# Optimization experiments

Hardware: AMD Instinct MI355X
Metric: run time of the kernel (lower is better)

Reference implementation:

```python
import jax, jax.numpy as jnp
import numpy as np

NEG_SLOPE = 0.2  # PyG GATConv default negative_slope


def setup_inputs() -> dict:
    key = jax.random.key(0)
    k1, k2, k3, k4, k5 = jax.random.split(key, 5)
    N, E, IN, H, C = 50000, 800000, 128, 4, 64
    x = jax.random.normal(k1, (N, IN), dtype=jnp.float32)
    edge_index = jax.random.randint(k2, (2, E), 0, N, dtype=jnp.int32)
    W = jax.random.normal(k3, (IN, H * C), dtype=jnp.float32) * (1.0 / np.sqrt(IN))
    att_src = jax.random.normal(k4, (H, C), dtype=jnp.float32) * 0.1
    att_dst = jax.random.normal(k5, (H, C), dtype=jnp.float32) * 0.1
    bias = jnp.zeros((C,), dtype=jnp.float32)
    return {"x": x, "edge_index": edge_index, "W": W,
            "att_src": att_src, "att_dst": att_dst, "bias": bias}


def reference(x, edge_index, W, att_src, att_dst, bias):
    N = x.shape[0]
    H, C = att_src.shape
    # add self loops (PyG GATConv default add_self_loops=True)
    loop = jnp.arange(N, dtype=edge_index.dtype)
    src = jnp.concatenate([edge_index[0], loop])  # message source j
    dst = jnp.concatenate([edge_index[1], loop])  # message target i
    # linear projection, per-head view [N, H, C]
    h = (x @ W).reshape(N, H, C)
    # per-node attention terms [N, H]
    a_src = jnp.einsum('nhc,hc->nh', h, att_src)
    a_dst = jnp.einsum('nhc,hc->nh', h, att_dst)
    # per-edge logits with leaky relu [Etot, H]
    e = jax.nn.leaky_relu(a_src[src] + a_dst[dst], NEG_SLOPE)
    # segment softmax over incoming edges of each destination node
    emax = jax.ops.segment_max(e, dst, num_segments=N)       # [N, H]
    ex = jnp.exp(e - emax[dst])                              # [Etot, H]
    denom = jax.ops.segment_sum(ex, dst, num_segments=N)     # [N, H]
    alpha = ex / denom[dst]                                  # [Etot, H]
    # weighted scatter-aggregate of source features
    msg = h[src] * alpha[:, :, None]                         # [Etot, H, C]
    out = jax.ops.segment_sum(msg, dst, num_segments=N)      # [N, H, C]
    # concat=False -> mean over heads, then bias, then module-level ELU
    out = out.mean(axis=1) + bias
    return jax.nn.elu(out)
```

## Files before the change

### kernel.cpp

```cpp
#include <hip/hip_runtime.h>

#define NEG_SLOPE 0.2f
static constexpr int IN_F = 128;
static constexpr int NHEAD = 4;
static constexpr int CH = 64;
static constexpr int HC = 256;
static constexpr int SC_EPB = 2000;
static constexpr int CB_CAP = 6144;

static __host__ size_t align256(size_t v) { return (v + 255) & ~((size_t)255); }

__device__ inline ushort f2bf(float f) {
    unsigned u = __float_as_uint(f);
    unsigned r = u + 0x7FFFu + ((u >> 16) & 1u);
    return (ushort)(r >> 16);
}
__device__ inline float bf2f(ushort s) { return __uint_as_float(((unsigned)s) << 16); }

typedef short s16x8 __attribute__((ext_vector_type(8)));
typedef float f32x16 __attribute__((ext_vector_type(16)));

__global__ __launch_bounds__(256) void prep_kernel(
    const float* __restrict__ W, ushort* __restrict__ Wt,
    int* __restrict__ coarse_cnt)
{
    int f = blockIdx.x * 256 + threadIdx.x;
    int k = f >> 8;
    int n = f & 255;
    Wt[n * IN_F + k] = f2bf(W[(size_t)k * HC + n]);
    if (blockIdx.x == 0) coarse_cnt[threadIdx.x] = 0;
}

__global__ __launch_bounds__(256) void gemm_mfma_kernel(
    const float* __restrict__ x, const ushort* __restrict__ Wt,
    const float* __restrict__ att_src, const float* __restrict__ att_dst,
    ushort* __restrict__ hb, float* __restrict__ a_src, float* __restrict__ a_dst,
    const int* __restrict__ dst, int* __restrict__ coarse_cnt,
    int E, int epb, int NTB, int NB, int N)
{
    constexpr int LDK = 136;
    __shared__ ushort As[64 * LDK];
    __shared__ ushort Bs[128 * LDK];
    ushort* Hs = As;

    const int t = threadIdx.x;

    if (blockIdx.x >= NTB) {
        int* hist = (int*)As;
        hist[t] = 0;
        __syncthreads();
        int slice = (blockIdx.x - NTB) * 2 + blockIdx.y;
        int lo = slice * epb;
        int hi = min(E, lo + epb);
        for (int i = lo + t; i < hi; i += 256)
            atomicAdd(&hist[((unsigned)dst[i]) >> 8], 1);
        __syncthreads();
        if (t < NB && hist[t]) atomicAdd(&coarse_cnt[t], hist[t]);
        return;
    }

    const int m0 = blockIdx.x * 64;
    const int n0 = blockIdx.y * 128;

    #pragma unroll
    for (int u = 0; u < 8; ++u) {
        int f = t + 256 * u;
        int r = f >> 5;
        int k4 = (f & 31) * 4;
        int row = m0 + r;
        float4 v = make_float4(0.f, 0.f, 0.f, 0.f);
        if (row < N) v = *(const float4*)(x + (size_t)row * IN_F + k4);
        ushort4 o;
        o.x = f2bf(v.x); o.y = f2bf(v.y); o.z = f2bf(v.z); o.w = f2bf(v.w);
        *(ushort4*)&As[r * LDK + k4] = o;
    }
    #pragma unroll
    for (int u = 0; u < 8; ++u) {
        int f = t + 256 * u;
        int n = f >> 4;
        int k8 = (f & 15) * 8;
        uint4 v = *(const uint4*)(Wt + (size_t)(n0 + n) * IN_F + k8);
        *(uint4*)&Bs[n * LDK + k8] = v;
    }
    __syncthreads();

    const int w = t >> 6;
    const int lane = t & 63;
    const int mrow = 32 * (w >> 1) + (lane & 31);
    const int nbase = 64 * (w & 1) + (lane & 31);
    const int kq = (lane >> 5) * 8;

    f32x16 acc0 = {}, acc1 = {};
    #pragma unroll
    for (int s = 0; s < 8; ++s) {
        s16x8 af = *(const s16x8*)&As[mrow * LDK + 16 * s + kq];
        s16x8 b0 = *(const s16x8*)&Bs[nbase * LDK + 16 * s + kq];
        s16x8 b1 = *(const s16x8*)&Bs[(nbase + 32) * LDK + 16 * s + kq];
        acc0 = __builtin_amdgcn_mfma_f32_32x32x16_bf16(af, b0, acc0, 0, 0, 0);
        acc1 = __builtin_amdgcn_mfma_f32_32x32x16_bf16(af, b1, acc1, 0, 0, 0);
    }
    __syncthreads();

    {
        int rbase = 4 * (lane >> 5) + 32 * (w >> 1);
        int c0 = 64 * (w & 1) + (lane & 31);
        #pragma unroll
        for (int r = 0; r < 16; ++r) {
            int rowL = rbase + (r & 3) + 8 * (r >> 2);
            Hs[rowL * LDK + c0]      = f2bf(acc0[r]);
            Hs[rowL * LDK + c0 + 32] = f2bf(acc1[r]);
        }
    }
    __syncthreads();

    {
        int r2 = t >> 2;
        int q = t & 3;
        int row = m0 + r2;
        uint4 p0 = *(const uint4*)&Hs[r2 * LDK + 32 * q];
        uint4 p1 = *(const uint4*)&Hs[r2 * LDK + 32 * q + 8];
        uint4 p2 = *(const uint4*)&Hs[r2 * LDK + 32 * q + 16];
        uint4 p3 = *(const uint4*)&Hs[r2 * LDK + 32 * q + 24];
        if (row < N) {
            ushort* dsth = hb + (size_t)row * HC + n0 + 32 * q;
            *(uint4*)(dsth)      = p0;
            *(uint4*)(dsth + 8)  = p1;
            *(uint4*)(dsth + 16) = p2;
            *(uint4*)(dsth + 24) = p3;
        }
        int hq = 2 * blockIdx.y + (q >> 1);
        int cb = (q & 1) * 32;
        const float* asp = att_src + hq * CH + cb;
        const float* adp = att_dst + hq * CH + cb;
        unsigned uu[16] = { p0.x, p0.y, p0.z, p0.w, p1.x, p1.y, p1.z, p1.w,
                            p2.x, p2.y, p2.z, p2.w, p3.x, p3.y, p3.z, p3.w };
        float ps = 0.f, pd = 0.f;
        #pragma unroll
        for (int i = 0; i < 16; ++i) {
            float lo = bf2f((ushort)(uu[i] & 0xFFFFu));
            float hi = bf2f((ushort)(uu[i] >> 16));
            ps += lo * asp[2 * i] + hi * asp[2 * i + 1];
            pd += lo * adp[2 * i] + hi * adp[2 * i + 1];
        }
        ps += __shfl_xor(ps, 1, 64);
        pd += __shfl_xor(pd, 1, 64);
        if ((q & 1) == 0 && row < N) {
            a_src[(size_t)row * NHEAD + hq] = ps;
            a_dst[(size_t)row * NHEAD + hq] = pd;
        }
    }
}

__global__ __launch_bounds__(256) void scan_coarse(
    const int* __restrict__ coarse_cnt, int* __restrict__ ebase,
    int* __restrict__ bucket_cur, int* __restrict__ rowptr,
    int NB, int N, int E)
{
    __shared__ int sm[256];
    int t = threadIdx.x;
    int v = (t < NB) ? coarse_cnt[t] : 0;
    sm[t] = v;
    __syncthreads();
    #pragma unroll
    for (int off = 1; off < 256; off <<= 1) {
        int a = sm[t];
        int b = (t >= off) ? sm[t - off] : 0;
        __syncthreads();
        sm[t] = a + b;
        __syncthreads();
    }
    int incl = sm[t];
    int excl = incl - v;
    if (t < NB) { ebase[t] = excl; bucket_cur[t] = excl; }
    if (t == NB - 1) ebase[NB] = incl;
    if (t == 0) rowptr[N] = E + N;
}

__global__ __launch_bounds__(256) void bucket_scatter(
    const int* __restrict__ src, const int* __restrict__ dst,
    int* __restrict__ bucket_cur, unsigned* __restrict__ ebuf,
    int E, int NB)
{
    __shared__ int hist[256];
    __shared__ int lbase[256];
    __shared__ int gbase[256];
    __shared__ int cur[256];
    __shared__ unsigned sbuf[SC_EPB + 48];
    __shared__ unsigned char tb[SC_EPB + 48];
    int t = threadIdx.x;
    int lo = blockIdx.x * SC_EPB;
    int hi = min(E, lo + SC_EPB);
    int cnt = hi - lo;
    hist[t] = 0;
    __syncthreads();
    unsigned pk[8]; int bk[8];
    #pragma unroll
    for (int u = 0; u < 8; ++u) {
        int i = lo + t + 256 * u;
        bk[u] = -1;
        if (i < hi) {
            unsigned d = (unsigned)dst[i];
            bk[u] = (int)(d >> 8);
            pk[u] = (((unsigned)src[i]) << 8) | (d & 255u);
            atomicAdd(&hist[bk[u]], 1);
        }
    }
    __syncthreads();
    int v = hist[t];
    lbase[t] = v;
    __syncthreads();
    #pragma unroll
    for (int off = 1; off < 256; off <<= 1) {
        int a = lbase[t];
        int b = (t >= off) ? lbase[t - off] : 0;
        __syncthreads();
        lbase[t] = a + b;
        __syncthreads();
    }
    int excl = lbase[t] - v;
    if (v) gbase[t] = atomicAdd(&bucket_cur[t], v);
    __syncthreads();
    lbase[t] = excl;
    cur[t] = excl;
    __syncthreads();
    #pragma unroll
    for (int u = 0; u < 8; ++u) {
        if (bk[u] >= 0) {
            int p = atomicAdd(&cur[bk[u]], 1);
            sbuf[p] = pk[u];
            tb[p] = (unsigned char)bk[u];
        }
    }
    __syncthreads();
    for (int j = t; j < cnt; j += 256) {
        int b = tb[j];
        ebuf[gbase[b] + j - lbase[b]] = sbuf[j];
    }
}

__global__ __launch_bounds__(256) void csr_build(
    const unsigned* __restrict__ ebuf, const int* __restrict__ ebase,
    int* __restrict__ rowptr, int* __restrict__ csr_src, int N)
{
    __shared__ int hist[256];
    __shared__ int scn[256];
    __shared__ int cur[256];
    __shared__ unsigned srt[CB_CAP];
    int b = blockIdx.x;
    int t = threadIdx.x;
    int n0 = b << 8;
    int ncnt = min(256, N - n0);
    int lo = ebase[b], hi = ebase[b + 1];
    int cnt = hi - lo;
    int cb = lo + n0;
    hist[t] = 0;
    __syncthreads();
    for (int i = lo + t; i < hi; i += 256)
        atomicAdd(&hist[ebuf[i] & 255u], 1);
    __syncthreads();
    int v = hist[t];
    scn[t] = v;
    __syncthreads();
    #pragma unroll
    for (int off = 1; off < 256; off <<= 1) {
        int a = scn[t];
        int bb = (t >= off) ? scn[t - off] : 0;
        __syncthreads();
        scn[t] = a + bb;
        __syncthreads();
    }
    int excl = scn[t] - v;
    if (t < ncnt) {
        int segstart = cb + excl + t;
        rowptr[n0 + t] = segstart;
        csr_src[segstart] = n0 + t;
    }
    cur[t] = excl;
    __syncthreads();
    if (cnt <= CB_CAP) {
        for (int i = lo + t; i < hi; i += 256) {
            unsigned e = ebuf[i];
            int p = atomicAdd(&cur[e & 255u], 1);
            srt[p] = e;
        }
        __syncthreads();
        for (int j = t; j < cnt; j += 256) {
            unsigned e = srt[j];
            csr_src[cb + j + (int)(e & 255u) + 1] = (int)(e >> 8);
        }
    } else {
        for (int i = lo + t; i < hi; i += 256) {
            unsigned e = ebuf[i];
            int ln = (int)(e & 255u);
            int p = atomicAdd(&cur[ln], 1);
            csr_src[cb + p + ln + 1] = (int)(e >> 8);
        }
    }
}

__global__ __launch_bounds__(256) void aggregate_kernel(
    const ushort* __restrict__ hb, const float* __restrict__ a_src,
    const float* __restrict__ a_dst, const int* __restrict__ rowptr,
    const int* __restrict__ csr_src, const float* __restrict__ bias,
    float* __restrict__ out, int N)
{
    int node = (int)((blockIdx.x * (size_t)blockDim.x + threadIdx.x) >> 6);
    int l = threadIdx.x & 63;
    if (node >= N) return;
    int start = rowptr[node];
    int end = rowptr[node + 1];
    int hd = l >> 4;
    float adh = a_dst[(size_t)node * NHEAD + hd];

    float4 acc0 = make_float4(0.f, 0.f, 0.f, 0.f);
    float4 acc1 = make_float4(0.f, 0.f, 0.f, 0.f);
    float4 acc2 = make_float4(0.f, 0.f, 0.f, 0.f);
    float4 acc3 = make_float4(0.f, 0.f, 0.f, 0.f);
    float s0 = 0.f, s1 = 0.f, s2 = 0.f, s3 = 0.f;

    int k = start;
    for (; k + 4 <= end; k += 4) {
        int sj0 = csr_src[k];
        int sj1 = csr_src[k + 1];
        int sj2 = csr_src[k + 2];
        int sj3 = csr_src[k + 3];
        float a0 = a_src[(size_t)sj0 * NHEAD + hd];
        float a1 = a_src[(size_t)sj1 * NHEAD + hd];
        float a2 = a_src[(size_t)sj2 * NHEAD + hd];
        float a3 = a_src[(size_t)sj3 * NHEAD + hd];
        ushort4 h0 = *(const ushort4*)(hb + ((size_t)sj0 << 8) + 4 * l);
        ushort4 h1 = *(const ushort4*)(hb + ((size_t)sj1 << 8) + 4 * l);
        ushort4 h2 = *(const ushort4*)(hb + ((size_t)sj2 << 8) + 4 * l);
        ushort4 h3 = *(const ushort4*)(hb + ((size_t)sj3 << 8) + 4 * l);
        float e0 = a0 + adh; e0 = fmaxf(e0, NEG_SLOPE * e0); float w0 = __expf(e0);
        float e1 = a1 + adh; e1 = fmaxf(e1, NEG_SLOPE * e1); float w1 = __expf(e1);
        float e2 = a2 + adh; e2 = fmaxf(e2, NEG_SLOPE * e2); float w2 = __expf(e2);
        float e3 = a3 + adh; e3 = fmaxf(e3, NEG_SLOPE * e3); float w3 = __expf(e3);
        s0 += w0; s1 += w1; s2 += w2; s3 += w3;
        acc0.x += w0 * bf2f(h0.x); acc0.y += w0 * bf2f(h0.y);
        acc0.z += w0 * bf2f(h0.z); acc0.w += w0 * bf2f(h0.w);
        acc1.x += w1 * bf2f(h1.x); acc1.y += w1 * bf2f(h1.y);
        acc1.z += w1 * bf2f(h1.z); acc1.w += w1 * bf2f(h1.w);
        acc2.x += w2 * bf2f(h2.x); acc2.y += w2 * bf2f(h2.y);
        acc2.z += w2 * bf2f(h2.z); acc2.w += w2 * bf2f(h2.w);
        acc3.x += w3 * bf2f(h3.x); acc3.y += w3 * bf2f(h3.y);
        acc3.z += w3 * bf2f(h3.z); acc3.w += w3 * bf2f(h3.w);
    }
    for (; k < end; ++k) {
        int sj0 = csr_src[k];
        float a0 = a_src[(size_t)sj0 * NHEAD + hd];
        ushort4 h0 = *(const ushort4*)(hb + ((size_t)sj0 << 8) + 4 * l);
        float e0 = a0 + adh; e0 = fmaxf(e0, NEG_SLOPE * e0);
        float w0 = __expf(e0);
        s0 += w0;
        acc0.x += w0 * bf2f(h0.x); acc0.y += w0 * bf2f(h0.y);
        acc0.z += w0 * bf2f(h0.z); acc0.w += w0 * bf2f(h0.w);
    }

    float inv = 1.0f / (s0 + s1 + s2 + s3);
    float4 acc;
    acc.x = (acc0.x + acc1.x + acc2.x + acc3.x) * inv;
    acc.y = (acc0.y + acc1.y + acc2.y + acc3.y) * inv;
    acc.z = (acc0.z + acc1.z + acc2.z + acc3.z) * inv;
    acc.w = (acc0.w + acc1.w + acc2.w + acc3.w) * inv;

    #pragma unroll
    for (int off = 16; off < 64; off <<= 1) {
        acc.x += __shfl_xor(acc.x, off, 64);
        acc.y += __shfl_xor(acc.y, off, 64);
        acc.z += __shfl_xor(acc.z, off, 64);
        acc.w += __shfl_xor(acc.w, off, 64);
    }
    if (l < 16) {
        float4 b4 = *(const float4*)(bias + 4 * l);
        float4 o;
        o.x = acc.x * 0.25f + b4.x;
        o.y = acc.y * 0.25f + b4.y;
        o.z = acc.z * 0.25f + b4.z;
        o.w = acc.w * 0.25f + b4.w;
        o.x = (o.x > 0.f) ? o.x : (__expf(o.x) - 1.f);
        o.y = (o.y > 0.f) ? o.y : (__expf(o.y) - 1.f);
        o.z = (o.z > 0.f) ? o.z : (__expf(o.z) - 1.f);
        o.w = (o.w > 0.f) ? o.w : (__expf(o.w) - 1.f);
        *(float4*)(out + (size_t)node * CH + 4 * l) = o;
    }
}

extern "C" void kernel_launch(void* const* d_in, const int* in_sizes, int n_in,
                              void* d_out, int out_size, void* d_ws, size_t ws_size,
                              hipStream_t stream)
{
    const float* x         = (const float*)d_in[0];
    const int*   edge_idx  = (const int*)d_in[1];
    const float* W         = (const float*)d_in[2];
    const float* att_src   = (const float*)d_in[3];
    const float* att_dst   = (const float*)d_in[4];
    const float* bias      = (const float*)d_in[5];
    float* out = (float*)d_out;

    const int N = in_sizes[0] / IN_F;
    const int E = in_sizes[1] / 2;
    const int Etot = E + N;
    const int NB = (N + 255) >> 8;
    const int* srcp = edge_idx;
    const int* dstp = edge_idx + E;

    char* ws = (char*)d_ws;
    size_t off = 0;
    ushort*  hb     = (ushort*)(ws + off);   off += align256((size_t)N * HC * sizeof(ushort));
    ushort*  Wt     = (ushort*)(ws + off);   off += align256((size_t)HC * IN_F * sizeof(ushort));
    float*   a_src  = (float*)(ws + off);    off += align256((size_t)N * NHEAD * sizeof(float));
    float*   a_dst  = (float*)(ws + off);    off += align256((size_t)N * NHEAD * sizeof(float));
    int*     ccnt   = (int*)(ws + off);      off += align256(256 * sizeof(int));
    int*     ebase  = (int*)(ws + off);      off += align256(257 * sizeof(int));
    int*     bcur   = (int*)(ws + off);      off += align256(256 * sizeof(int));
    unsigned* ebuf  = (unsigned*)(ws + off); off += align256((size_t)E * sizeof(unsigned));
    int*     rowptr = (int*)(ws + off);      off += align256(((size_t)N + 1) * sizeof(int));
    int*     csrs   = (int*)(ws + off);      off += align256((size_t)Etot * sizeof(int));
    (void)ws_size; (void)n_in; (void)out_size;

    const int NTB = (N + 63) / 64;
    const int PBC = 208;
    const int epbc = (E + 2 * PBC - 1) / (2 * PBC);
    const int PBS = (E + SC_EPB - 1) / SC_EPB;

    prep_kernel<<<IN_F * HC / 256, 256, 0, stream>>>(W, Wt, ccnt);
    dim3 gg(NTB + PBC, 2);
    gemm_mfma_kernel<<<gg, 256, 0, stream>>>(x, Wt, att_src, att_dst, hb,
                                             a_src, a_dst, dstp, ccnt,
                                             E, epbc, NTB, NB, N);
    scan_coarse<<<1, 256, 0, stream>>>(ccnt, ebase, bcur, rowptr, NB, N, E);
    bucket_scatter<<<PBS, 256, 0, stream>>>(srcp, dstp, bcur, ebuf, E, NB);
    csr_build<<<NB, 256, 0, stream>>>(ebuf, ebase, rowptr, csrs, N);
    aggregate_kernel<<<((size_t)N * 64 + 255) / 256, 256, 0, stream>>>(
        hb, a_src, a_dst, rowptr, csrs, bias, out, N);
}
```

Before: 203.8 us.

## Precompute fp16 edge attention weights in CSR build and drop scan kernel

Removes the single-block scan_coarse launch by having bucket_scatter and csr_build each redo the 256-entry scan of the coarse counts. csr_build now also computes each edge's exponentiated leaky-relu logits for all four heads, stores them as fp16 alongside csr_src, and accumulates per-node softmax denominators with shared atomics, writing their reciprocals. The aggregate kernel then reads precomputed weights and the inverse denominator instead of gathering a_src and computing exp per edge per lane. This trades a launch and redundant exp work for an extra 8-byte-per-edge weight array and shared float atomics. It also adds fp16 precision risk, since there is no max subtraction and exp values could overflow fp16.

```diff
diff --git a/kernel.cpp b/kernel.cpp
--- a/kernel.cpp
+++ b/kernel.cpp
@@ -16,19 +16,32 @@
     return (ushort)(r >> 16);
 }
 __device__ inline float bf2f(ushort s) { return __uint_as_float(((unsigned)s) << 16); }
+__device__ inline ushort f2h(float f) {
+    _Float16 h = (_Float16)f;
+    return *(ushort*)&h;
+}
+__device__ inline float h2f(ushort u) {
+    _Float16 h = *(_Float16*)&u;
+    return (float)h;
+}
 
 typedef short s16x8 __attribute__((ext_vector_type(8)));
 typedef float f32x16 __attribute__((ext_vector_type(16)));
 
 __global__ __launch_bounds__(256) void prep_kernel(
     const float* __restrict__ W, ushort* __restrict__ Wt,
-    int* __restrict__ coarse_cnt)
+    int* __restrict__ ccnt, int* __restrict__ cur0,
+    int* __restrict__ rowptr, int N, int Etot)
 {
     int f = blockIdx.x * 256 + threadIdx.x;
     int k = f >> 8;
     int n = f & 255;
     Wt[n * IN_F + k] = f2bf(W[(size_t)k * HC + n]);
-    if (blockIdx.x == 0) coarse_cnt[threadIdx.x] = 0;
+    if (blockIdx.x == 0) {
+        ccnt[threadIdx.x] = 0;
+        cur0[threadIdx.x] = 0;
+        if (threadIdx.x == 0) rowptr[N] = Etot;
+    }
 }
 
 __global__ __launch_bounds__(256) void gemm_mfma_kernel(
@@ -151,36 +164,12 @@
     }
 }
 
-__global__ __launch_bounds__(256) void scan_coarse(
-    const int* __restrict__ coarse_cnt, int* __restrict__ ebase,
-    int* __restrict__ bucket_cur, int* __restrict__ rowptr,
-    int NB, int N, int E)
-{
-    __shared__ int sm[256];
-    int t = threadIdx.x;
-    int v = (t < NB) ? coarse_cnt[t] : 0;
-    sm[t] = v;
-    __syncthreads();
-    #pragma unroll
-    for (int off = 1; off < 256; off <<= 1) {
-        int a = sm[t];
-        int b = (t >= off) ? sm[t - off] : 0;
-        __syncthreads();
-        sm[t] = a + b;
-        __syncthreads();
-    }
-    int incl = sm[t];
-    int excl = incl - v;
-    if (t < NB) { ebase[t] = excl; bucket_cur[t] = excl; }
-    if (t == NB - 1) ebase[NB] = incl;
-    if (t == 0) rowptr[N] = E + N;
-}
-
 __global__ __launch_bounds__(256) void bucket_scatter(
     const int* __restrict__ src, const int* __restrict__ dst,
-    int* __restrict__ bucket_cur, unsigned* __restrict__ ebuf,
-    int E, int NB)
+    const int* __restrict__ ccnt, int* __restrict__ cur0,
+    unsigned* __restrict__ ebuf, int E)
 {
+    __shared__ int eb[256];
     __shared__ int hist[256];
     __shared__ int lbase[256];
     __shared__ int gbase[256];
@@ -188,6 +177,21 @@
     __shared__ unsigned sbuf[SC_EPB + 48];
     __shared__ unsigned char tb[SC_EPB + 48];
     int t = threadIdx.x;
+    int cv = ccnt[t];
+    eb[t] = cv;
+    __syncthreads();
+    #pragma unroll
+    for (int off = 1; off < 256; off <<= 1) {
+        int a = eb[t];
+        int b = (t >= off) ? eb[t - off] : 0;
+        __syncthreads();
+        eb[t] = a + b;
+        __syncthreads();
+    }
+    int myebase = eb[t] - cv;
+    __syncthreads();
+    eb[t] = myebase;
+
     int lo = blockIdx.x * SC_EPB;
     int hi = min(E, lo + SC_EPB);
     int cnt = hi - lo;
@@ -218,7 +222,7 @@
         __syncthreads();
     }
     int excl = lbase[t] - v;
-    if (v) gbase[t] = atomicAdd(&bucket_cur[t], v);
+    if (v) gbase[t] = eb[t] + atomicAdd(&cur0[t], v);
     __syncthreads();
     lbase[t] = excl;
     cur[t] = excl;
@@ -239,27 +243,21 @@
 }
 
 __global__ __launch_bounds__(256) void csr_build(
-    const unsigned* __restrict__ ebuf, const int* __restrict__ ebase,
-    int* __restrict__ rowptr, int* __restrict__ csr_src, int N)
+    const unsigned* __restrict__ ebuf, const int* __restrict__ ccnt,
+    const float* __restrict__ a_src, const float* __restrict__ a_dst,
+    int* __restrict__ rowptr, int* __restrict__ csr_src,
+    ushort* __restrict__ csr_w, float* __restrict__ dinv, int N, int NB)
 {
+    __shared__ int scn[256];
     __shared__ int hist[256];
-    __shared__ int scn[256];
     __shared__ int cur[256];
     __shared__ unsigned srt[CB_CAP];
+    __shared__ float4 adl[256];
+    __shared__ float denom[256][4];
     int b = blockIdx.x;
     int t = threadIdx.x;
-    int n0 = b << 8;
-    int ncnt = min(256, N - n0);
-    int lo = ebase[b], hi = ebase[b + 1];
-    int cnt = hi - lo;
-    int cb = lo + n0;
-    hist[t] = 0;
-    __syncthreads();
-    for (int i = lo + t; i < hi; i += 256)
-        atomicAdd(&hist[ebuf[i] & 255u], 1);
-    __syncthreads();
-    int v = hist[t];
-    scn[t] = v;
+    int cv = ccnt[t];
+    scn[t] = cv;
     __syncthreads();
     #pragma unroll
     for (int off = 1; off < 256; off <<= 1) {
@@ -269,11 +267,50 @@
         scn[t] = a + bb;
         __syncthreads();
     }
+    int lo = (b == 0) ? 0 : scn[b - 1];
+    int hi = scn[b];
+    __syncthreads();
+
+    int n0 = b << 8;
+    int ncnt = min(256, N - n0);
+    int cnt = hi - lo;
+    int cb = lo + n0;
+
+    if (t < ncnt) adl[t] = *(const float4*)(a_dst + (size_t)(n0 + t) * NHEAD);
+    denom[t][0] = 0.f; denom[t][1] = 0.f; denom[t][2] = 0.f; denom[t][3] = 0.f;
+    hist[t] = 0;
+    __syncthreads();
+    for (int i = lo + t; i < hi; i += 256)
+        atomicAdd(&hist[ebuf[i] & 255u], 1);
+    __syncthreads();
+    int v = hist[t];
+    scn[t] = v;
+    __syncthreads();
+    #pragma unroll
+    for (int off = 1; off < 256; off <<= 1) {
+        int a = scn[t];
+        int bb = (t >= off) ? scn[t - off] : 0;
+        __syncthreads();
+        scn[t] = a + bb;
+        __syncthreads();
+    }
     int excl = scn[t] - v;
     if (t < ncnt) {
-        int segstart = cb + excl + t;
-        rowptr[n0 + t] = segstart;
-        csr_src[segstart] = n0 + t;
+        int seg = cb + excl + t;
+        rowptr[n0 + t] = seg;
+        csr_src[seg] = n0 + t;
+        float4 as4 = *(const float4*)(a_src + (size_t)(n0 + t) * NHEAD);
+        float4 ad4 = adl[t];
+        float e0 = as4.x + ad4.x; e0 = fmaxf(e0, NEG_SLOPE * e0);
+        float e1 = as4.y + ad4.y; e1 = fmaxf(e1, NEG_SLOPE * e1);
+        float e2 = as4.z + ad4.z; e2 = fmaxf(e2, NEG_SLOPE * e2);
+        float e3 = as4.w + ad4.w; e3 = fmaxf(e3, NEG_SLOPE * e3);
+        ushort4 pw;
+        pw.x = f2h(__expf(e0)); pw.y = f2h(__expf(e1));
+        pw.z = f2h(__expf(e2)); pw.w = f2h(__expf(e3));
+        *(ushort4*)(csr_w + (size_t)seg * 4) = pw;
+        denom[t][0] += h2f(pw.x); denom[t][1] += h2f(pw.y);
+        denom[t][2] += h2f(pw.z); denom[t][3] += h2f(pw.w);
     }
     cur[t] = excl;
     __syncthreads();
@@ -286,22 +323,64 @@
         __syncthreads();
         for (int j = t; j < cnt; j += 256) {
             unsigned e = srt[j];
-            csr_src[cb + j + (int)(e & 255u) + 1] = (int)(e >> 8);
+            int ln = (int)(e & 255u);
+            int s = (int)(e >> 8);
+            float4 as4 = *(const float4*)(a_src + (size_t)s * NHEAD);
+            float4 ad4 = adl[ln];
+            float e0 = as4.x + ad4.x; e0 = fmaxf(e0, NEG_SLOPE * e0);
+            float e1 = as4.y + ad4.y; e1 = fmaxf(e1, NEG_SLOPE * e1);
+            float e2 = as4.z + ad4.z; e2 = fmaxf(e2, NEG_SLOPE * e2);
+            float e3 = as4.w + ad4.w; e3 = fmaxf(e3, NEG_SLOPE * e3);
+            ushort4 pw;
+            pw.x = f2h(__expf(e0)); pw.y = f2h(__expf(e1));
+            pw.z = f2h(__expf(e2)); pw.w = f2h(__expf(e3));
+            int slot = cb + j + ln + 1;
+            csr_src[slot] = s;
+            *(ushort4*)(csr_w + (size_t)slot * 4) = pw;
+            atomicAdd(&denom[ln][0], h2f(pw.x));
+            atomicAdd(&denom[ln][1], h2f(pw.y));
+            atomicAdd(&denom[ln][2], h2f(pw.z));
+            atomicAdd(&denom[ln][3], h2f(pw.w));
         }
     } else {
         for (int i = lo + t; i < hi; i += 256) {
             unsigned e = ebuf[i];
             int ln = (int)(e & 255u);
+            int s = (int)(e >> 8);
             int p = atomicAdd(&cur[ln], 1);
-            csr_src[cb + p + ln + 1] = (int)(e >> 8);
-        }
+            float4 as4 = *(const float4*)(a_src + (size_t)s * NHEAD);
+            float4 ad4 = adl[ln];
+            float e0 = as4.x + ad4.x; e0 = fmaxf(e0, NEG_SLOPE * e0);
+            float e1 = as4.y + ad4.y; e1 = fmaxf(e1, NEG_SLOPE * e1);
+            float e2 = as4.z + ad4.z; e2 = fmaxf(e2, NEG_SLOPE * e2);
+            float e3 = as4.w + ad4.w; e3 = fmaxf(e3, NEG_SLOPE * e3);
+            ushort4 pw;
+            pw.x = f2h(__expf(e0)); pw.y = f2h(__expf(e1));
+            pw.z = f2h(__expf(e2)); pw.w = f2h(__expf(e3));
+            int slot = cb + p + ln + 1;
+            csr_src[slot] = s;
+            *(ushort4*)(csr_w + (size_t)slot * 4) = pw;
+            atomicAdd(&denom[ln][0], h2f(pw.x));
+            atomicAdd(&denom[ln][1], h2f(pw.y));
+            atomicAdd(&denom[ln][2], h2f(pw.z));
+            atomicAdd(&denom[ln][3], h2f(pw.w));
+        }
+    }
+    __syncthreads();
+    if (t < ncnt) {
+        float4 dv;
+        dv.x = 1.0f / denom[t][0];
+        dv.y = 1.0f / denom[t][1];
+        dv.z = 1.0f / denom[t][2];
+        dv.w = 1.0f / denom[t][3];
+        *(float4*)(dinv + (size_t)(n0 + t) * NHEAD) = dv;
     }
 }
 
 __global__ __launch_bounds__(256) void aggregate_kernel(
-    const ushort* __restrict__ hb, const float* __restrict__ a_src,
-    const float* __restrict__ a_dst, const int* __restrict__ rowptr,
-    const int* __restrict__ csr_src, const float* __restrict__ bias,
+    const ushort* __restrict__ hb, const int* __restrict__ rowptr,
+    const int* __restrict__ csr_src, const ushort* __restrict__ csr_w,
+    const float* __restrict__ dinv, const float* __restrict__ bias,
     float* __restrict__ out, int N)
 {
     int node = (int)((blockIdx.x * (size_t)blockDim.x + threadIdx.x) >> 6);
@@ -310,13 +389,11 @@
     int start = rowptr[node];
     int end = rowptr[node + 1];
     int hd = l >> 4;
-    float adh = a_dst[(size_t)node * NHEAD + hd];
 
     float4 acc0 = make_float4(0.f, 0.f, 0.f, 0.f);
     float4 acc1 = make_float4(0.f, 0.f, 0.f, 0.f);
     float4 acc2 = make_float4(0.f, 0.f, 0.f, 0.f);
     float4 acc3 = make_float4(0.f, 0.f, 0.f, 0.f);
-    float s0 = 0.f, s1 = 0.f, s2 = 0.f, s3 = 0.f;
 
     int k = start;
     for (; k + 4 <= end; k += 4) {
@@ -324,19 +401,22 @@
         int sj1 = csr_src[k + 1];
         int sj2 = csr_src[k + 2];
         int sj3 = csr_src[k + 3];
-        float a0 = a_src[(size_t)sj0 * NHEAD + hd];
-        float a1 = a_src[(size_t)sj1 * NHEAD + hd];
-        float a2 = a_src[(size_t)sj2 * NHEAD + hd];
-        float a3 = a_src[(size_t)sj3 * NHEAD + hd];
+        uint2 wv0 = *(const uint2*)(csr_w + (size_t)(k + 0) * 4);
+        uint2 wv1 = *(const uint2*)(csr_w + (size_t)(k + 1) * 4);
+        uint2 wv2 = *(const uint2*)(csr_w + (size_t)(k + 2) * 4);
+        uint2 wv3 = *(const uint2*)(csr_w + (size_t)(k + 3) * 4);
         ushort4 h0 = *(const ushort4*)(hb + ((size_t)sj0 << 8) + 4 * l);
         ushort4 h1 = *(const ushort4*)(hb + ((size_t)sj1 << 8) + 4 * l);
         ushort4 h2 = *(const ushort4*)(hb + ((size_t)sj2 << 8) + 4 * l);
         ushort4 h3 = *(const ushort4*)(hb + ((size_t)sj3 << 8) + 4 * l);
-        float e0 = a0 + adh; e0 = fmaxf(e0, NEG_SLOPE * e0); float w0 = __expf(e0);
-        float e1 = a1 + adh; e1 = fmaxf(e1, NEG_SLOPE * e1); float w1 = __expf(e1);
-        float e2 = a2 + adh; e2 = fmaxf(e2, NEG_SLOPE * e2); float w2 = __expf(e2);
-        float e3 = a3 + adh; e3 = fmaxf(e3, NEG_SLOPE * e3); float w3 = __expf(e3);
-        s0 += w0; s1 += w1; s2 += w2; s3 += w3;
+        unsigned d0 = (hd & 2) ? wv0.y : wv0.x;
+        unsigned d1 = (hd & 2) ? wv1.y : wv1.x;
+        unsigned d2 = (hd & 2) ? wv2.y : wv2.x;
+        unsigned d3 = (hd & 2) ? wv3.y : wv3.x;
+        float w0 = h2f((ushort)((hd & 1) ? (d0 >> 16) : (d0 & 0xFFFFu)));
+        float w1 = h2f((ushort)((hd & 1) ? (d1 >> 16) : (d1 & 0xFFFFu)));
+        float w2 = h2f((ushort)((hd & 1) ? (d2 >> 16) : (d2 & 0xFFFFu)));
+        float w3 = h2f((ushort)((hd & 1) ? (d3 >> 16) : (d3 & 0xFFFFu)));
         acc0.x += w0 * bf2f(h0.x); acc0.y += w0 * bf2f(h0.y);
         acc0.z += w0 * bf2f(h0.z); acc0.w += w0 * bf2f(h0.w);
         acc1.x += w1 * bf2f(h1.x); acc1.y += w1 * bf2f(h1.y);
@@ -348,16 +428,15 @@
     }
     for (; k < end; ++k) {
         int sj0 = csr_src[k];
-        float a0 = a_src[(size_t)sj0 * NHEAD + hd];
+        uint2 wv0 = *(const uint2*)(csr_w + (size_t)k * 4);
         ushort4 h0 = *(const ushort4*)(hb + ((size_t)sj0 << 8) + 4 * l);
-        float e0 = a0 + adh; e0 = fmaxf(e0, NEG_SLOPE * e0);
-        float w0 = __expf(e0);
-        s0 += w0;
+        unsigned d0 = (hd & 2) ? wv0.y : wv0.x;
+        float w0 = h2f((ushort)((hd & 1) ? (d0 >> 16) : (d0 & 0xFFFFu)));
         acc0.x += w0 * bf2f(h0.x); acc0.y += w0 * bf2f(h0.y);
         acc0.z += w0 * bf2f(h0.z); acc0.w += w0 * bf2f(h0.w);
     }
 
-    float inv = 1.0f / (s0 + s1 + s2 + s3);
+    float inv = dinv[(size_t)node * NHEAD + hd];
     float4 acc;
     acc.x = (acc0.x + acc1.x + acc2.x + acc3.x) * inv;
     acc.y = (acc0.y + acc1.y + acc2.y + acc3.y) * inv;
@@ -412,11 +491,12 @@
     float*   a_src  = (float*)(ws + off);    off += align256((size_t)N * NHEAD * sizeof(float));
     float*   a_dst  = (float*)(ws + off);    off += align256((size_t)N * NHEAD * sizeof(float));
     int*     ccnt   = (int*)(ws + off);      off += align256(256 * sizeof(int));
-    int*     ebase  = (int*)(ws + off);      off += align256(257 * sizeof(int));
-    int*     bcur   = (int*)(ws + off);      off += align256(256 * sizeof(int));
+    int*     cur0   = (int*)(ws + off);      off += align256(256 * sizeof(int));
     unsigned* ebuf  = (unsigned*)(ws + off); off += align256((size_t)E * sizeof(unsigned));
     int*     rowptr = (int*)(ws + off);      off += align256(((size_t)N + 1) * sizeof(int));
     int*     csrs   = (int*)(ws + off);      off += align256((size_t)Etot * sizeof(int));
+    ushort*  csr_w  = (ushort*)(ws + off);   off += align256((size_t)Etot * NHEAD * sizeof(ushort));
+    float*   dinv   = (float*)(ws + off);    off += align256((size_t)N * NHEAD * sizeof(float));
     (void)ws_size; (void)n_in; (void)out_size;
 
     const int NTB = (N + 63) / 64;
@@ -424,14 +504,14 @@
     const int epbc = (E + 2 * PBC - 1) / (2 * PBC);
     const int PBS = (E + SC_EPB - 1) / SC_EPB;
 
-    prep_kernel<<<IN_F * HC / 256, 256, 0, stream>>>(W, Wt, ccnt);
+    prep_kernel<<<IN_F * HC / 256, 256, 0, stream>>>(W, Wt, ccnt, cur0, rowptr, N, Etot);
     dim3 gg(NTB + PBC, 2);
     gemm_mfma_kernel<<<gg, 256, 0, stream>>>(x, Wt, att_src, att_dst, hb,
                                              a_src, a_dst, dstp, ccnt,
                                              E, epbc, NTB, NB, N);
-    scan_coarse<<<1, 256, 0, stream>>>(ccnt, ebase, bcur, rowptr, NB, N, E);
-    bucket_scatter<<<PBS, 256, 0, stream>>>(srcp, dstp, bcur, ebuf, E, NB);
-    csr_build<<<NB, 256, 0, stream>>>(ebuf, ebase, rowptr, csrs, N);
+    bucket_scatter<<<PBS, 256, 0, stream>>>(srcp, dstp, ccnt, cur0, ebuf, E);
+    csr_build<<<NB, 256, 0, stream>>>(ebuf, ccnt, a_src, a_dst,
+                                      rowptr, csrs, csr_w, dinv, N, NB);
     aggregate_kernel<<<((size_t)N * 64 + 255) / 256, 256, 0, stream>>>(
-        hb, a_src, a_dst, rowptr, csrs, bias, out, N);
-}
+        hb, rowptr, csrs, csr_w, dinv, bias, out, N);
+}
```

New measurement: 232.2 us. +13.9%, slower.

## Fold coarse scan into consumers and split each node's edges across two waves

Applied to the files above, without the earlier changes.

Drops the single-block scan_coarse launch: bucket_scatter and csr_build now each redo the 256-entry prefix scan of the coarse counts themselves, and prep zeroes a separate cursor array and writes rowptr[N]. The aggregate kernel now assigns two wavefronts per destination node, each handling half the edge list, and combines the partial sums and softmax denominators through shared memory before normalising and writing. This removes one kernel launch and its serialisation, and doubles the wave-level parallelism in aggregation. The cost is a redundant scan in every block, plus an extra __syncthreads and a shared-memory reduction in aggregation.

```diff
diff --git a/kernel.cpp b/kernel.cpp
--- a/kernel.cpp
+++ b/kernel.cpp
@@ -22,13 +22,18 @@
 
 __global__ __launch_bounds__(256) void prep_kernel(
     const float* __restrict__ W, ushort* __restrict__ Wt,
-    int* __restrict__ coarse_cnt)
+    int* __restrict__ ccnt, int* __restrict__ cur0,
+    int* __restrict__ rowptr, int N, int Etot)
 {
     int f = blockIdx.x * 256 + threadIdx.x;
     int k = f >> 8;
     int n = f & 255;
     Wt[n * IN_F + k] = f2bf(W[(size_t)k * HC + n]);
-    if (blockIdx.x == 0) coarse_cnt[threadIdx.x] = 0;
+    if (blockIdx.x == 0) {
+        ccnt[threadIdx.x] = 0;
+        cur0[threadIdx.x] = 0;
+        if (threadIdx.x == 0) rowptr[N] = Etot;
+    }
 }
 
 __global__ __launch_bounds__(256) void gemm_mfma_kernel(
@@ -151,36 +156,12 @@
     }
 }
 
-__global__ __launch_bounds__(256) void scan_coarse(
-    const int* __restrict__ coarse_cnt, int* __restrict__ ebase,
-    int* __restrict__ bucket_cur, int* __restrict__ rowptr,
-    int NB, int N, int E)
-{
-    __shared__ int sm[256];
-    int t = threadIdx.x;
-    int v = (t < NB) ? coarse_cnt[t] : 0;
-    sm[t] = v;
-    __syncthreads();
-    #pragma unroll
-    for (int off = 1; off < 256; off <<= 1) {
-        int a = sm[t];
-        int b = (t >= off) ? sm[t - off] : 0;
-        __syncthreads();
-        sm[t] = a + b;
-        __syncthreads();
-    }
-    int incl = sm[t];
-    int excl = incl - v;
-    if (t < NB) { ebase[t] = excl; bucket_cur[t] = excl; }
-    if (t == NB - 1) ebase[NB] = incl;
-    if (t == 0) rowptr[N] = E + N;
-}
-
 __global__ __launch_bounds__(256) void bucket_scatter(
     const int* __restrict__ src, const int* __restrict__ dst,
-    int* __restrict__ bucket_cur, unsigned* __restrict__ ebuf,
-    int E, int NB)
-{
+    const int* __restrict__ ccnt, int* __restrict__ cur0,
+    unsigned* __restrict__ ebuf, int E)
+{
+    __shared__ int eb[256];
     __shared__ int hist[256];
     __shared__ int lbase[256];
     __shared__ int gbase[256];
@@ -188,6 +169,21 @@
     __shared__ unsigned sbuf[SC_EPB + 48];
     __shared__ unsigned char tb[SC_EPB + 48];
     int t = threadIdx.x;
+    int cv = ccnt[t];
+    eb[t] = cv;
+    __syncthreads();
+    #pragma unroll
+    for (int off = 1; off < 256; off <<= 1) {
+        int a = eb[t];
+        int b = (t >= off) ? eb[t - off] : 0;
+        __syncthreads();
+        eb[t] = a + b;
+        __syncthreads();
+    }
+    int myebase = eb[t] - cv;
+    __syncthreads();
+    eb[t] = myebase;
+
     int lo = blockIdx.x * SC_EPB;
     int hi = min(E, lo + SC_EPB);
     int cnt = hi - lo;
@@ -218,7 +214,7 @@
         __syncthreads();
     }
     int excl = lbase[t] - v;
-    if (v) gbase[t] = atomicAdd(&bucket_cur[t], v);
+    if (v) gbase[t] = eb[t] + atomicAdd(&cur0[t], v);
     __syncthreads();
     lbase[t] = excl;
     cur[t] = excl;
@@ -239,18 +235,32 @@
 }
 
 __global__ __launch_bounds__(256) void csr_build(
-    const unsigned* __restrict__ ebuf, const int* __restrict__ ebase,
+    const unsigned* __restrict__ ebuf, const int* __restrict__ ccnt,
     int* __restrict__ rowptr, int* __restrict__ csr_src, int N)
 {
+    __shared__ int scn[256];
     __shared__ int hist[256];
-    __shared__ int scn[256];
     __shared__ int cur[256];
     __shared__ unsigned srt[CB_CAP];
     int b = blockIdx.x;
     int t = threadIdx.x;
+    int cv = ccnt[t];
+    scn[t] = cv;
+    __syncthreads();
+    #pragma unroll
+    for (int off = 1; off < 256; off <<= 1) {
+        int a = scn[t];
+        int bb = (t >= off) ? scn[t - off] : 0;
+        __syncthreads();
+        scn[t] = a + bb;
+        __syncthreads();
+    }
+    int lo = (b == 0) ? 0 : scn[b - 1];
+    int hi = scn[b];
+    __syncthreads();
+
     int n0 = b << 8;
     int ncnt = min(256, N - n0);
-    int lo = ebase[b], hi = ebase[b + 1];
     int cnt = hi - lo;
     int cb = lo + n0;
     hist[t] = 0;
@@ -304,13 +314,27 @@
     const int* __restrict__ csr_src, const float* __restrict__ bias,
     float* __restrict__ out, int N)
 {
-    int node = (int)((blockIdx.x * (size_t)blockDim.x + threadIdx.x) >> 6);
-    int l = threadIdx.x & 63;
-    if (node >= N) return;
-    int start = rowptr[node];
-    int end = rowptr[node + 1];
+    __shared__ float accsm[2][64][4];
+    __shared__ float ssm[2][4];
+    int t = threadIdx.x;
+    int w = t >> 6;
+    int half = w & 1;
+    int lnode = w >> 1;
+    int node = blockIdx.x * 2 + lnode;
+    int l = t & 63;
     int hd = l >> 4;
-    float adh = a_dst[(size_t)node * NHEAD + hd];
+
+    bool active = node < N;
+    int start = 0, end = 0;
+    float adh = 0.f;
+    if (active) {
+        start = rowptr[node];
+        end = rowptr[node + 1];
+        adh = a_dst[(size_t)node * NHEAD + hd];
+    }
+    int hdeg = (end - start + 1) >> 1;
+    int mylo = start + half * hdeg;
+    int myhi = half ? end : (start + hdeg);
 
     float4 acc0 = make_float4(0.f, 0.f, 0.f, 0.f);
     float4 acc1 = make_float4(0.f, 0.f, 0.f, 0.f);
@@ -318,8 +342,8 @@
     float4 acc3 = make_float4(0.f, 0.f, 0.f, 0.f);
     float s0 = 0.f, s1 = 0.f, s2 = 0.f, s3 = 0.f;
 
-    int k = start;
-    for (; k + 4 <= end; k += 4) {
+    int k = mylo;
+    for (; k + 4 <= myhi; k += 4) {
         int sj0 = csr_src[k];
         int sj1 = csr_src[k + 1];
         int sj2 = csr_src[k + 2];
@@ -346,7 +370,7 @@
         acc3.x += w3 * bf2f(h3.x); acc3.y += w3 * bf2f(h3.y);
         acc3.z += w3 * bf2f(h3.z); acc3.w += w3 * bf2f(h3.w);
     }
-    for (; k < end; ++k) {
+    for (; k < myhi; ++k) {
         int sj0 = csr_src[k];
         float a0 = a_src[(size_t)sj0 * NHEAD + hd];
         ushort4 h0 = *(const ushort4*)(hb + ((size_t)sj0 << 8) + 4 * l);
@@ -357,32 +381,43 @@
         acc0.z += w0 * bf2f(h0.z); acc0.w += w0 * bf2f(h0.w);
     }
 
-    float inv = 1.0f / (s0 + s1 + s2 + s3);
     float4 acc;
-    acc.x = (acc0.x + acc1.x + acc2.x + acc3.x) * inv;
-    acc.y = (acc0.y + acc1.y + acc2.y + acc3.y) * inv;
-    acc.z = (acc0.z + acc1.z + acc2.z + acc3.z) * inv;
-    acc.w = (acc0.w + acc1.w + acc2.w + acc3.w) * inv;
-
-    #pragma unroll
-    for (int off = 16; off < 64; off <<= 1) {
-        acc.x += __shfl_xor(acc.x, off, 64);
-        acc.y += __shfl_xor(acc.y, off, 64);
-        acc.z += __shfl_xor(acc.z, off, 64);
-        acc.w += __shfl_xor(acc.w, off, 64);
-    }
-    if (l < 16) {
-        float4 b4 = *(const float4*)(bias + 4 * l);
-        float4 o;
-        o.x = acc.x * 0.25f + b4.x;
-        o.y = acc.y * 0.25f + b4.y;
-        o.z = acc.z * 0.25f + b4.z;
-        o.w = acc.w * 0.25f + b4.w;
-        o.x = (o.x > 0.f) ? o.x : (__expf(o.x) - 1.f);
-        o.y = (o.y > 0.f) ? o.y : (__expf(o.y) - 1.f);
-        o.z = (o.z > 0.f) ? o.z : (__expf(o.z) - 1.f);
-        o.w = (o.w > 0.f) ? o.w : (__expf(o.w) - 1.f);
-        *(float4*)(out + (size_t)node * CH + 4 * l) = o;
+    acc.x = acc0.x + acc1.x + acc2.x + acc3.x;
+    acc.y = acc0.y + acc1.y + acc2.y + acc3.y;
+    acc.z = acc0.z + acc1.z + acc2.z + acc3.z;
+    acc.w = acc0.w + acc1.w + acc2.w + acc3.w;
+    float sloc = s0 + s1 + s2 + s3;
+
+    if (half == 1) {
+        *(float4*)&accsm[lnode][l][0] = acc;
+        if ((l & 15) == 0) ssm[lnode][hd] = sloc;
+    }
+    __syncthreads();
+    if (half == 0 && active) {
+        float4 o2 = *(const float4*)&accsm[lnode][l][0];
+        acc.x += o2.x; acc.y += o2.y; acc.z += o2.z; acc.w += o2.w;
+        float inv = 1.0f / (sloc + ssm[lnode][hd]);
+        acc.x *= inv; acc.y *= inv; acc.z *= inv; acc.w *= inv;
+        #pragma unroll
+        for (int off = 16; off < 64; off <<= 1) {
+            acc.x += __shfl_xor(acc.x, off, 64);
+            acc.y += __shfl_xor(acc.y, off, 64);
+            acc.z += __shfl_xor(acc.z, off, 64);
+            acc.w += __shfl_xor(acc.w, off, 64);
+        }
+        if (l < 16) {
+            float4 b4 = *(const float4*)(bias + 4 * l);
+            float4 o;
+            o.x = acc.x * 0.25f + b4.x;
+            o.y = acc.y * 0.25f + b4.y;
+            o.z = acc.z * 0.25f + b4.z;
+            o.w = acc.w * 0.25f + b4.w;
+            o.x = (o.x > 0.f) ? o.x : (__expf(o.x) - 1.f);
+            o.y = (o.y > 0.f) ? o.y : (__expf(o.y) - 1.f);
+            o.z = (o.z > 0.f) ? o.z : (__expf(o.z) - 1.f);
+            o.w = (o.w > 0.f) ? o.w : (__expf(o.w) - 1.f);
+            *(float4*)(out + (size_t)node * CH + 4 * l) = o;
+        }
     }
 }
 
@@ -412,8 +447,7 @@
     float*   a_src  = (float*)(ws + off);    off += align256((size_t)N * NHEAD * sizeof(float));
     float*   a_dst  = (float*)(ws + off);    off += align256((size_t)N * NHEAD * sizeof(float));
     int*     ccnt   = (int*)(ws + off);      off += align256(256 * sizeof(int));
-    int*     ebase  = (int*)(ws + off);      off += align256(257 * sizeof(int));
-    int*     bcur   = (int*)(ws + off);      off += align256(256 * sizeof(int));
+    int*     cur0   = (int*)(ws + off);      off += align256(256 * sizeof(int));
     unsigned* ebuf  = (unsigned*)(ws + off); off += align256((size_t)E * sizeof(unsigned));
     int*     rowptr = (int*)(ws + off);      off += align256(((size_t)N + 1) * sizeof(int));
     int*     csrs   = (int*)(ws + off);      off += align256((size_t)Etot * sizeof(int));
@@ -424,14 +458,13 @@
     const int epbc = (E + 2 * PBC - 1) / (2 * PBC);
     const int PBS = (E + SC_EPB - 1) / SC_EPB;
 
-    prep_kernel<<<IN_F * HC / 256, 256, 0, stream>>>(W, Wt, ccnt);
+    prep_kernel<<<IN_F * HC / 256, 256, 0, stream>>>(W, Wt, ccnt, cur0, rowptr, N, Etot);
     dim3 gg(NTB + PBC, 2);
     gemm_mfma_kernel<<<gg, 256, 0, stream>>>(x, Wt, att_src, att_dst, hb,
                                              a_src, a_dst, dstp, ccnt,
                                              E, epbc, NTB, NB, N);
-    scan_coarse<<<1, 256, 0, stream>>>(ccnt, ebase, bcur, rowptr, NB, N, E);
-    bucket_scatter<<<PBS, 256, 0, stream>>>(srcp, dstp, bcur, ebuf, E, NB);
-    csr_build<<<NB, 256, 0, stream>>>(ebuf, ebase, rowptr, csrs, N);
-    aggregate_kernel<<<((size_t)N * 64 + 255) / 256, 256, 0, stream>>>(
+    bucket_scatter<<<PBS, 256, 0, stream>>>(srcp, dstp, ccnt, cur0, ebuf, E);
+    csr_build<<<NB, 256, 0, stream>>>(ebuf, ccnt, rowptr, csrs, N);
+    aggregate_kernel<<<((N + 1) / 2), 256, 0, stream>>>(
         hb, a_src, a_dst, rowptr, csrs, bias, out, N);
 }
```

After: 207.3 us. No clear change (+1.7%).
